# Kernel tuning notes

Hardware: AMD Instinct MI355X
Metric: run time of the kernel (lower is better)

The kernel has to match this reference:

```python
import jax, jax.numpy as jnp
import numpy as np

N_NODES = 100000
N_EDGES = 1600000
IN_DIM = 128
HID = 64      # gat_hidden
HEADS = 4
D = HID // HEADS  # per-head out_dim = 16
EPS = 1e-9
NEG_SLOPE = 0.2


def setup_inputs() -> dict:
    key = jax.random.key(0)
    ks = jax.random.split(key, 10)
    x = jax.random.normal(ks[0], (N_NODES, IN_DIM), dtype=jnp.float32)
    edge_index = jax.random.randint(ks[1], (2, N_EDGES), 0, N_NODES, dtype=jnp.int32)
    # node_embed: Linear(IN_DIM, HID) + ReLU (dropout = identity in eval)
    w_embed = jax.random.normal(ks[2], (IN_DIM, HID), dtype=jnp.float32) * 0.08
    b_embed = jnp.zeros((HID,), dtype=jnp.float32)
    # two GAT layers: lin (HID -> HEADS*D, no bias), att_src/att_dst [HEADS, D]
    lin_w0 = jax.random.normal(ks[3], (HID, HEADS * D), dtype=jnp.float32) * 0.12
    att_src0 = jax.random.normal(ks[4], (HEADS, D), dtype=jnp.float32) * 0.25
    att_dst0 = jax.random.normal(ks[5], (HEADS, D), dtype=jnp.float32) * 0.25
    lin_w1 = jax.random.normal(ks[6], (HID, HEADS * D), dtype=jnp.float32) * 0.12
    att_src1 = jax.random.normal(ks[7], (HEADS, D), dtype=jnp.float32) * 0.25
    att_dst1 = jax.random.normal(ks[8], (HEADS, D), dtype=jnp.float32) * 0.25
    return {
        "x": x, "w_embed": w_embed, "b_embed": b_embed,
        "lin_w0": lin_w0, "att_src0": att_src0, "att_dst0": att_dst0,
        "lin_w1": lin_w1, "att_src1": att_src1, "att_dst1": att_dst1,
        "edge_index": edge_index,
    }


def _gat_layer(h, src, dst, lin_w, att_src, att_dst):
    # h: [N, HID] -> out: [N, HEADS*D]
    n = h.shape[0]
    xp = (h @ lin_w).reshape(n, HEADS, D)          # [N, H, D]
    x_j = xp[src]                                   # source (neighbor) feats [E, H, D]
    x_i = xp[dst]                                   # destination feats      [E, H, D]
    e = (x_j * att_src).sum(-1) + (x_i * att_dst).sum(-1)   # [E, H]
    e = jnp.where(e > 0, e, NEG_SLOPE * e)          # LeakyReLU(0.2)
    exp_e = jnp.exp(e)                              # unnormalized, matches original (no max-subtract)
    denom = jax.ops.segment_sum(exp_e, dst, num_segments=n)  # [N, H]
    alpha = exp_e / (denom[dst] + EPS)              # [E, H]
    out = jax.ops.segment_sum(x_j * alpha[:, :, None], dst, num_segments=n)  # [N, H, D]
    return out.reshape(n, HEADS * D)


def reference(x, w_embed, b_embed, lin_w0, att_src0, att_dst0,
              lin_w1, att_src1, att_dst1, edge_index):
    src, dst = edge_index[0], edge_index[1]
    h = jax.nn.relu(x @ w_embed + b_embed)          # node_embed (eval: dropout = id)
    h = _gat_layer(h, src, dst, lin_w0, att_src0, att_dst0)
    h = _gat_layer(h, src, dst, lin_w1, att_src1, att_dst1)
    return jax.nn.relu(h)                            # gat_post (eval)
```

## Files before the change

kernel.cpp:

```cpp
#include <hip/hip_runtime.h>
#include <hip/hip_bf16.h>

#define N_HEADS 4
#define HID 64
#define IN_DIM 128
#define EPS 1e-9f
#define NEG_SLOPE 0.2f
#define CAP 48
#define NRANGE 8

typedef int   v4i __attribute__((ext_vector_type(4)));
typedef float v4f __attribute__((ext_vector_type(4)));

__global__ void __launch_bounds__(256) scatter_kernel(
        const int* __restrict__ src, const int* __restrict__ dst,
        int* __restrict__ cnt, int* __restrict__ csr, int E, int N) {
    int r = blockIdx.x & (NRANGE - 1);
    int i4 = (blockIdx.x >> 3) * blockDim.x + threadIdx.x;
    int range = (N + NRANGE - 1) / NRANGE;
    int lo = r * range;
    int hi = lo + range; hi = hi < N ? hi : N;
    int nq = E >> 2;
    if (i4 >= nq) return;
    int4 d4 = ((const int4*)dst)[i4];
    int ebase = i4 * 4;
    int dd[4] = {d4.x, d4.y, d4.z, d4.w};
    #pragma unroll
    for (int q = 0; q < 4; ++q) {
        int d = dd[q];
        if (d >= lo && d < hi) {
            int p = atomicAdd(&cnt[d], 1);
            if (p < CAP) csr[(size_t)d * CAP + p] = src[ebase + q];
        }
    }
}

__device__ __forceinline__ void linatt_phase(
        const float (*hs)[HID], int base,
        const float* __restrict__ lw,
        const float* __restrict__ att_s, const float* __restrict__ att_d,
        __hip_bfloat16* __restrict__ xpb, float* __restrict__ asrc,
        float* __restrict__ adst, int N) {
    int wv = threadIdx.x >> 6;
    int j  = threadIdx.x & 63;
    int n0 = base + wv * 4;
    float acc[4] = {0.f, 0.f, 0.f, 0.f};
    const float (*hr)[HID] = &hs[wv * 4];
    #pragma unroll 2
    for (int k = 0; k < HID; k += 4) {
        float4 h0v = *(const float4*)(&hr[0][k]);
        float4 h1v = *(const float4*)(&hr[1][k]);
        float4 h2v = *(const float4*)(&hr[2][k]);
        float4 h3v = *(const float4*)(&hr[3][k]);
        float w0 = lw[(k + 0) * HID + j];
        float w1 = lw[(k + 1) * HID + j];
        float w2 = lw[(k + 2) * HID + j];
        float w3 = lw[(k + 3) * HID + j];
        acc[0] = fmaf(h0v.x, w0, acc[0]); acc[0] = fmaf(h0v.y, w1, acc[0]);
        acc[0] = fmaf(h0v.z, w2, acc[0]); acc[0] = fmaf(h0v.w, w3, acc[0]);
        acc[1] = fmaf(h1v.x, w0, acc[1]); acc[1] = fmaf(h1v.y, w1, acc[1]);
        acc[1] = fmaf(h1v.z, w2, acc[1]); acc[1] = fmaf(h1v.w, w3, acc[1]);
        acc[2] = fmaf(h2v.x, w0, acc[2]); acc[2] = fmaf(h2v.y, w1, acc[2]);
        acc[2] = fmaf(h2v.z, w2, acc[2]); acc[2] = fmaf(h2v.w, w3, acc[2]);
        acc[3] = fmaf(h3v.x, w0, acc[3]); acc[3] = fmaf(h3v.y, w1, acc[3]);
        acc[3] = fmaf(h3v.z, w2, acc[3]); acc[3] = fmaf(h3v.w, w3, acc[3]);
    }
    float as = att_s[j], adw = att_d[j];
    #pragma unroll
    for (int q = 0; q < 4; ++q) {
        if (n0 + q >= N) break;
        float a = acc[q];
        xpb[(size_t)(n0 + q) * HID + j] = __float2bfloat16(a);
        float vs = a * as;
        float vd = a * adw;
        #pragma unroll
        for (int off = 8; off > 0; off >>= 1) {
            vs += __shfl_down(vs, off, 16);
            vd += __shfl_down(vd, off, 16);
        }
        if ((j & 15) == 0) {
            asrc[(size_t)(n0 + q) * N_HEADS + (j >> 4)] = vs;
            adst[(size_t)(n0 + q) * N_HEADS + (j >> 4)] = vd;
        }
    }
}

__global__ void __launch_bounds__(256) embed_linatt_kernel(
        const float* __restrict__ x, const float* __restrict__ w,
        const float* __restrict__ b, const float* __restrict__ lw,
        const float* __restrict__ att_s, const float* __restrict__ att_d,
        __hip_bfloat16* __restrict__ xpb, float* __restrict__ asrc,
        float* __restrict__ adst, int N) {
    __shared__ float xs[16][IN_DIM];
    __shared__ float hs[16][HID];
    int base = blockIdx.x * 16;
    int wv = threadIdx.x >> 6;
    int j  = threadIdx.x & 63;
    const v4f* xg = (const v4f*)(x + ((size_t)base + wv * 4) * IN_DIM);
    #pragma unroll
    for (int i = 0; i < 2; ++i) {
        int f4 = i * 64 + j;
        int row = f4 >> 5;
        int nn = base + wv * 4 + row;
        v4f v = (nn < N) ? xg[f4] : (v4f)0.f;
        *((v4f*)&xs[wv * 4 + row][(f4 & 31) * 4]) = v;
    }
    {
        float acc[4] = {0.f, 0.f, 0.f, 0.f};
        const float (*xr)[IN_DIM] = &xs[wv * 4];
        #pragma unroll 2
        for (int k = 0; k < IN_DIM; k += 4) {
            float4 v0 = *(const float4*)(&xr[0][k]);
            float4 v1 = *(const float4*)(&xr[1][k]);
            float4 v2 = *(const float4*)(&xr[2][k]);
            float4 v3 = *(const float4*)(&xr[3][k]);
            float w0 = w[(k + 0) * HID + j];
            float w1 = w[(k + 1) * HID + j];
            float w2 = w[(k + 2) * HID + j];
            float w3 = w[(k + 3) * HID + j];
            acc[0] = fmaf(v0.x, w0, acc[0]); acc[0] = fmaf(v0.y, w1, acc[0]);
            acc[0] = fmaf(v0.z, w2, acc[0]); acc[0] = fmaf(v0.w, w3, acc[0]);
            acc[1] = fmaf(v1.x, w0, acc[1]); acc[1] = fmaf(v1.y, w1, acc[1]);
            acc[1] = fmaf(v1.z, w2, acc[1]); acc[1] = fmaf(v1.w, w3, acc[1]);
            acc[2] = fmaf(v2.x, w0, acc[2]); acc[2] = fmaf(v2.y, w1, acc[2]);
            acc[2] = fmaf(v2.z, w2, acc[2]); acc[2] = fmaf(v2.w, w3, acc[2]);
            acc[3] = fmaf(v3.x, w0, acc[3]); acc[3] = fmaf(v3.y, w1, acc[3]);
            acc[3] = fmaf(v3.z, w2, acc[3]); acc[3] = fmaf(v3.w, w3, acc[3]);
        }
        float bb = b[j];
        #pragma unroll
        for (int q = 0; q < 4; ++q)
            hs[wv * 4 + q][j] = fmaxf(acc[q] + bb, 0.f);
    }
    linatt_phase(hs, base, lw, att_s, att_d, xpb, asrc, adst, N);
}

template <int WRITE_LDS>
__device__ __forceinline__ void agg_octet(
        int base, int N,
        const int* __restrict__ cnt, const int* __restrict__ csr,
        const float* __restrict__ asrc, const float* __restrict__ adst,
        const __hip_bfloat16* __restrict__ xpb,
        float (*hs)[HID], float* __restrict__ out) {
    int wv = threadIdx.x >> 6;
    int lane = threadIdx.x & 63;
    int eg = lane >> 2, hh = lane & 3;
    int k4 = (lane >> 3) << 2;
    int b  = lane & 7;
    int kb4H = k4 + (b >> 1);

    #pragma unroll
    for (int rr = 0; rr < 4; ++rr) {
        int nid = base + wv * 4 + rr;
        int node = nid < N ? nid : N - 1;
        int deg = cnt[node];
        deg = deg < CAP ? deg : CAP;
        if (nid >= N) deg = 0;
        const int* bucket = csr + (size_t)node * CAP;
        float adA = adst[(unsigned)node * N_HEADS + (unsigned)hh];
        int ng = (deg + 15) >> 4;
        float acc[8] = {0.f, 0.f, 0.f, 0.f, 0.f, 0.f, 0.f, 0.f};
        float wsum = 0.f;
        for (int g = 0; g < ng; ++g) {
            int t = g * 16 + eg;
            int raw = bucket[t];
            unsigned s = (t < deg) ? (unsigned)raw : 0u;
            float e = asrc[s * N_HEADS + (unsigned)hh] + adA;
            e = fmaxf(e, NEG_SLOPE * e);
            float w = (t < deg) ? __expf(e) : 0.f;
            #pragma unroll
            for (int p = 0; p < 2; ++p) {
                unsigned s_k = (unsigned)__shfl((int)s, k4 + p * 32, 64);
                float    w_k = __shfl(w, kb4H + p * 32, 64);
                uint4 v = *(const uint4*)(xpb + (size_t)s_k * HID + b * 8);
                acc[0] = fmaf(w_k, __uint_as_float(v.x << 16),          acc[0]);
                acc[1] = fmaf(w_k, __uint_as_float(v.x & 0xffff0000u),  acc[1]);
                acc[2] = fmaf(w_k, __uint_as_float(v.y << 16),          acc[2]);
                acc[3] = fmaf(w_k, __uint_as_float(v.y & 0xffff0000u),  acc[3]);
                acc[4] = fmaf(w_k, __uint_as_float(v.z << 16),          acc[4]);
                acc[5] = fmaf(w_k, __uint_as_float(v.z & 0xffff0000u),  acc[5]);
                acc[6] = fmaf(w_k, __uint_as_float(v.w << 16),          acc[6]);
                acc[7] = fmaf(w_k, __uint_as_float(v.w & 0xffff0000u),  acc[7]);
                wsum += w_k;
            }
        }
        #pragma unroll
        for (int i = 0; i < 8; ++i) acc[i] += __shfl_down(acc[i], 8, 64);
        wsum += __shfl_down(wsum, 8, 64);
        #pragma unroll
        for (int i = 0; i < 8; ++i) acc[i] += __shfl_down(acc[i], 16, 64);
        wsum += __shfl_down(wsum, 16, 64);
        #pragma unroll
        for (int i = 0; i < 8; ++i) acc[i] += __shfl_down(acc[i], 32, 64);
        wsum += __shfl_down(wsum, 32, 64);

        if (lane < 8 && nid < N) {
            float inv = 1.f / (wsum + EPS);
            if (WRITE_LDS) {
                v4f lo = {acc[0] * inv, acc[1] * inv, acc[2] * inv, acc[3] * inv};
                v4f hi = {acc[4] * inv, acc[5] * inv, acc[6] * inv, acc[7] * inv};
                *((v4f*)&hs[wv * 4 + rr][lane * 8])     = lo;
                *((v4f*)&hs[wv * 4 + rr][lane * 8 + 4]) = hi;
            } else {
                float* op = out + (size_t)nid * HID + lane * 8;
                v4f lo = {fmaxf(acc[0] * inv, 0.f), fmaxf(acc[1] * inv, 0.f),
                          fmaxf(acc[2] * inv, 0.f), fmaxf(acc[3] * inv, 0.f)};
                v4f hi = {fmaxf(acc[4] * inv, 0.f), fmaxf(acc[5] * inv, 0.f),
                          fmaxf(acc[6] * inv, 0.f), fmaxf(acc[7] * inv, 0.f)};
                *(v4f*)op = lo;
                *(v4f*)(op + 4) = hi;
            }
        }
    }
}

__global__ void __launch_bounds__(256) agg_linatt_kernel(
        const int* __restrict__ cnt, const int* __restrict__ csr,
        const float* __restrict__ asrc0, const float* __restrict__ adst0,
        const __hip_bfloat16* __restrict__ xpb0,
        const float* __restrict__ lw, const float* __restrict__ att_s,
        const float* __restrict__ att_d,
        __hip_bfloat16* __restrict__ xpb1, float* __restrict__ asrc1,
        float* __restrict__ adst1, int N) {
    __shared__ float hs[16][HID];
    int base = blockIdx.x * 16;
    agg_octet<1>(base, N, cnt, csr, asrc0, adst0, xpb0, hs, nullptr);
    linatt_phase(hs, base, lw, att_s, att_d, xpb1, asrc1, adst1, N);
}

__global__ void __launch_bounds__(256) agg_kernel(
        const int* __restrict__ cnt, const int* __restrict__ csr,
        const float* __restrict__ asrc, const float* __restrict__ adst,
        const __hip_bfloat16* __restrict__ xpb, float* __restrict__ out, int N) {
    int base = blockIdx.x * 16;
    agg_octet<0>(base, N, cnt, csr, asrc, adst, xpb, nullptr, out);
}

extern "C" void kernel_launch(void* const* d_in, const int* in_sizes, int n_in,
                              void* d_out, int out_size, void* d_ws, size_t ws_size,
                              hipStream_t stream) {
    const float* x       = (const float*)d_in[0];
    const float* w_embed = (const float*)d_in[1];
    const float* b_embed = (const float*)d_in[2];
    const float* lin_w0  = (const float*)d_in[3];
    const float* att_s0  = (const float*)d_in[4];
    const float* att_d0  = (const float*)d_in[5];
    const float* lin_w1  = (const float*)d_in[6];
    const float* att_s1  = (const float*)d_in[7];
    const float* att_d1  = (const float*)d_in[8];
    const int*   ei      = (const int*)d_in[9];

    const int N = in_sizes[0] / IN_DIM;
    const int E = in_sizes[9] / 2;
    const int* src = ei;
    const int* dst = ei + E;

    float* ws    = (float*)d_ws;
    float* asrc0 = ws;
    float* adst0 = asrc0 + (size_t)N * N_HEADS;
    float* asrc1 = adst0 + (size_t)N * N_HEADS;
    float* adst1 = asrc1 + (size_t)N * N_HEADS;
    int*   cnt   = (int*)(adst1 + (size_t)N * N_HEADS);
    int*   csr   = cnt + N;
    __hip_bfloat16* xpb0 = (__hip_bfloat16*)(csr + (size_t)N * CAP);
    __hip_bfloat16* xpb1 = xpb0 + (size_t)N * HID;
    float* outp = (float*)d_out;

    int blk16 = (N + 15) / 16;
    int sc_blocks = ((E / 4 + 255) / 256) * NRANGE;

    hipMemsetAsync(cnt, 0, (size_t)N * sizeof(int), stream);

    scatter_kernel<<<sc_blocks, 256, 0, stream>>>(src, dst, cnt, csr, E, N);

    embed_linatt_kernel<<<blk16, 256, 0, stream>>>(
        x, w_embed, b_embed, lin_w0, att_s0, att_d0, xpb0, asrc0, adst0, N);

    agg_linatt_kernel<<<blk16, 256, 0, stream>>>(
        cnt, csr, asrc0, adst0, xpb0, lin_w1, att_s1, att_d1, xpb1, asrc1, adst1, N);

    agg_kernel<<<blk16, 256, 0, stream>>>(cnt, csr, asrc1, adst1, xpb1, outp, N);
}
```

Baseline: 246.6 us.

## Fuse CSR scatter and embed/linear-attention into one interleaved-block kernel

New measurement: 208.1 us (median of 2 runs). -15.6%, faster.

```diff
diff --git a/kernel.cpp b/kernel.cpp
--- a/kernel.cpp
+++ b/kernel.cpp
@@ -11,29 +11,6 @@
 
 typedef int   v4i __attribute__((ext_vector_type(4)));
 typedef float v4f __attribute__((ext_vector_type(4)));
-
-__global__ void __launch_bounds__(256) scatter_kernel(
-        const int* __restrict__ src, const int* __restrict__ dst,
-        int* __restrict__ cnt, int* __restrict__ csr, int E, int N) {
-    int r = blockIdx.x & (NRANGE - 1);
-    int i4 = (blockIdx.x >> 3) * blockDim.x + threadIdx.x;
-    int range = (N + NRANGE - 1) / NRANGE;
-    int lo = r * range;
-    int hi = lo + range; hi = hi < N ? hi : N;
-    int nq = E >> 2;
-    if (i4 >= nq) return;
-    int4 d4 = ((const int4*)dst)[i4];
-    int ebase = i4 * 4;
-    int dd[4] = {d4.x, d4.y, d4.z, d4.w};
-    #pragma unroll
-    for (int q = 0; q < 4; ++q) {
-        int d = dd[q];
-        if (d >= lo && d < hi) {
-            int p = atomicAdd(&cnt[d], 1);
-            if (p < CAP) csr[(size_t)d * CAP + p] = src[ebase + q];
-        }
-    }
-}
 
 __device__ __forceinline__ void linatt_phase(
         const float (*hs)[HID], int base,
@@ -85,15 +62,44 @@
     }
 }
 
-__global__ void __launch_bounds__(256) embed_linatt_kernel(
+__global__ void __launch_bounds__(256) scatter_embed_kernel(
+        const int* __restrict__ src, const int* __restrict__ dst,
+        int* __restrict__ cnt, int* __restrict__ csr, int E, int N,
         const float* __restrict__ x, const float* __restrict__ w,
         const float* __restrict__ b, const float* __restrict__ lw,
         const float* __restrict__ att_s, const float* __restrict__ att_d,
         __hip_bfloat16* __restrict__ xpb, float* __restrict__ asrc,
-        float* __restrict__ adst, int N) {
+        float* __restrict__ adst) {
     __shared__ float xs[16][IN_DIM];
     __shared__ float hs[16][HID];
-    int base = blockIdx.x * 16;
+    int B = blockIdx.x;
+    int m = B % 24;
+    if (m % 3 != 2) {
+        int r = B & 7;
+        int occ = (0x6D9200u >> m) & 1;
+        int seq = (B / 24) * 2 + occ;
+        int i4 = seq * 256 + (int)threadIdx.x;
+        int range = (N + NRANGE - 1) / NRANGE;
+        int lo = r * range;
+        int hi = lo + range; hi = hi < N ? hi : N;
+        int nq = E >> 2;
+        if (i4 >= nq) return;
+        int4 d4 = ((const int4*)dst)[i4];
+        int ebase = i4 * 4;
+        int dd[4] = {d4.x, d4.y, d4.z, d4.w};
+        #pragma unroll
+        for (int q = 0; q < 4; ++q) {
+            int d = dd[q];
+            if (d >= lo && d < hi) {
+                int p = atomicAdd(&cnt[d], 1);
+                if (p < CAP) csr[(size_t)d * CAP + p] = src[ebase + q];
+            }
+        }
+        return;
+    }
+    int eidx = B / 3;
+    int base = eidx * 16;
+    if (base >= N) return;
     int wv = threadIdx.x >> 6;
     int j  = threadIdx.x & 63;
     const v4f* xg = (const v4f*)(x + ((size_t)base + wv * 4) * IN_DIM);
@@ -267,14 +273,18 @@
     float* outp = (float*)d_out;
 
     int blk16 = (N + 15) / 16;
-    int sc_blocks = ((E / 4 + 255) / 256) * NRANGE;
+    int nq = E >> 2;
+    int seqs = (nq + 255) / 256;
+    int g_sc = (seqs + 1) / 2;
+    int g_em = (blk16 + 7) / 8;
+    int groups = g_sc > g_em ? g_sc : g_em;
+    int fused_blocks = groups * 24;
 
     hipMemsetAsync(cnt, 0, (size_t)N * sizeof(int), stream);
 
-    scatter_kernel<<<sc_blocks, 256, 0, stream>>>(src, dst, cnt, csr, E, N);
-
-    embed_linatt_kernel<<<blk16, 256, 0, stream>>>(
-        x, w_embed, b_embed, lin_w0, att_s0, att_d0, xpb0, asrc0, adst0, N);
+    scatter_embed_kernel<<<fused_blocks, 256, 0, stream>>>(
+        src, dst, cnt, csr, E, N,
+        x, w_embed, b_embed, lin_w0, att_s0, att_d0, xpb0, asrc0, adst0);
 
     agg_linatt_kernel<<<blk16, 256, 0, stream>>>(
         cnt, csr, asrc0, adst0, xpb0, lin_w1, att_s1, att_d1, xpb1, asrc1, adst1, N);
```
